# Kernel tuning notes

Hardware: AMD Instinct MI355X
Metric: run time of the kernel (lower is better)

The kernel has to match this reference:

```python
import jax, jax.numpy as jnp
import numpy as np

N_HEADS = 32
N_KV_HEADS = 8
HEAD_DIM = 128
HIDDEN = 4096
ROPE_BASE = 10000.0


def _rope_tables(seq_len, head_dim, base):
    inv_freq = 1.0 / (base ** (jnp.arange(0, head_dim, 2, dtype=jnp.float32) / head_dim))
    t = jnp.arange(seq_len, dtype=jnp.float32)
    freqs = jnp.outer(t, inv_freq)                    # (S, D/2)
    emb = jnp.concatenate([freqs, freqs], axis=-1)    # (S, D)
    return jnp.cos(emb), jnp.sin(emb)


def _rotate_half(x):
    half = x.shape[-1] // 2
    return jnp.concatenate([-x[..., half:], x[..., :half]], axis=-1)


def _apply_rope(x, cos, sin):
    # x: (B, H, S, D); cos/sin: (S, D)
    return x * cos[None, None] + _rotate_half(x) * sin[None, None]


def setup_inputs() -> dict:
    key = jax.random.key(0)
    k1, k2, k3 = jax.random.split(key, 3)
    bsz, q_len = 2, 2048
    total_heads = N_HEADS + 2 * N_KV_HEADS
    hidden_states = jax.random.normal(k1, (bsz, q_len, HIDDEN), dtype=jnp.float32)
    w_qkv = jax.random.normal(k2, (total_heads * HEAD_DIM, HIDDEN), dtype=jnp.float32) * 0.02
    w_o = jax.random.normal(k3, (HIDDEN, N_HEADS * HEAD_DIM), dtype=jnp.float32) * 0.02
    return {"hidden_states": hidden_states, "w_qkv": w_qkv, "w_o": w_o}


def reference(hidden_states, w_qkv, w_o):
    bsz, q_len, _ = hidden_states.shape
    n_rep = N_HEADS // N_KV_HEADS

    qkv = jnp.einsum('bsh,oh->bso', hidden_states, w_qkv)  # (B, S, total_heads*D)
    q_sz = N_HEADS * HEAD_DIM
    kv_sz = N_KV_HEADS * HEAD_DIM
    q = qkv[..., :q_sz].reshape(bsz, q_len, N_HEADS, HEAD_DIM).transpose(0, 2, 1, 3)
    k = qkv[..., q_sz:q_sz + kv_sz].reshape(bsz, q_len, N_KV_HEADS, HEAD_DIM).transpose(0, 2, 1, 3)
    v = qkv[..., q_sz + kv_sz:].reshape(bsz, q_len, N_KV_HEADS, HEAD_DIM).transpose(0, 2, 1, 3)

    cos, sin = _rope_tables(q_len, HEAD_DIM, ROPE_BASE)
    q = _apply_rope(q, cos, sin)
    k = _apply_rope(k, cos, sin)

    # repeat KV heads for GQA
    k = jnp.repeat(k, n_rep, axis=1)  # (B, H, S, D)
    v = jnp.repeat(v, n_rep, axis=1)

    scale = HEAD_DIM ** -0.5
    scores = jnp.einsum('bhqd,bhkd->bhqk', q, k) * scale
    causal = jnp.tril(jnp.ones((q_len, q_len), dtype=bool))
    scores = jnp.where(causal[None, None], scores, jnp.finfo(scores.dtype).min)
    attn = jax.nn.softmax(scores, axis=-1)
    out = jnp.einsum('bhqk,bhkd->bhqd', attn, v)  # (B, H, S, D)
    out = out.transpose(0, 2, 1, 3).reshape(bsz, q_len, N_HEADS * HEAD_DIM)
    return jnp.einsum('bso,ho->bsh', out, w_o)
```

## Files before the change

### kernel.cpp

```cpp
#include <hip/hip_runtime.h>
#include <stdint.h>

#define N_HEADS   32
#define N_KV      8
#define HEAD_DIM  128
#define HIDDEN_DIM 4096
#define BSZ       2
#define SEQ       2048
#define TOT_HEADS 48
#define QKV_DIM   6144
#define ROWS      4096
#define ROPE_HEADS 40

typedef __attribute__((ext_vector_type(4)))  float f32x4;
typedef __attribute__((ext_vector_type(16))) float f32x16;
typedef __attribute__((ext_vector_type(8)))  short bf16x8;
typedef unsigned short u16;
typedef unsigned int   u32;

#define AS1 __attribute__((address_space(1)))
#define AS3 __attribute__((address_space(3)))

static __device__ __forceinline__ float bf16f(u16 u) { return __uint_as_float(((u32)u) << 16); }
static __device__ __forceinline__ u16 f2bf(float f) {
  u32 x = __float_as_uint(f);
  x += 0x7fffu + ((x >> 16) & 1u);
  return (u16)(x >> 16);
}
static __device__ __forceinline__ u32 cvt_pk_bf16(float lo, float hi) {
  u32 r;
  asm("v_cvt_pk_bf16_f32 %0, %1, %2" : "=v"(r) : "v"(lo), "v"(hi));
  return r;
}
static __device__ __forceinline__ bf16x8 mk8(u32 a, u32 b, u32 c, u32 d) {
  union { u32 u[4]; bf16x8 v; } x;
  x.u[0] = a; x.u[1] = b; x.u[2] = c; x.u[3] = d;
  return x.v;
}

__global__ void cast_f32_bf16_k(const float4* __restrict__ in, ushort4* __restrict__ out, int n4) {
  int i = blockIdx.x * blockDim.x + threadIdx.x;
  const int stride = gridDim.x * blockDim.x;
  for (; i < n4; i += stride) {
    float4 v = in[i];
    ushort4 o;
    o.x = f2bf(v.x); o.y = f2bf(v.y); o.z = f2bf(v.z); o.w = f2bf(v.w);
    out[i] = o;
  }
}

__global__ void rope_tables_k(float* __restrict__ ctab, float* __restrict__ stab) {
  int t = blockIdx.x * blockDim.x + threadIdx.x;
  if (t >= SEQ * 64) return;
  int s = t >> 6, i = t & 63;
  float inv = powf(10000.0f, -(float)i / 64.0f);
  float ang = (float)s * inv;
  float sv, cv;
  sincosf(ang, &sv, &cv);
  ctab[t] = cv; stab[t] = sv;
}

template<int F32OUT>
__global__ __launch_bounds__(256, 2)
void gemm_bt_k(const u16* __restrict__ A, const u16* __restrict__ Bw,
               void* __restrict__ C, int M, int N, int K)
{
  __shared__ uint4 smA[1024];
  __shared__ uint4 smB[1024];
  const int tid = threadIdx.x;
  const int nbx = N >> 7;
  const int bm = (blockIdx.x / nbx) << 7;
  const int bn = (blockIdx.x % nbx) << 7;
  const int lane = tid & 63;
  const int wave = tid >> 6;
  const int wm = (wave >> 1) << 6;
  const int wn = (wave & 1) << 6;
  const int fr = lane & 15;
  const int fq = lane >> 4;

  f32x4 acc[4][4];
#pragma unroll
  for (int i = 0; i < 4; ++i)
#pragma unroll
    for (int j = 0; j < 4; ++j)
      acc[i][j] = {0.f, 0.f, 0.f, 0.f};

  const int gl_r = lane >> 3;
  const int gl_c = (lane & 7) ^ gl_r;

  for (int k0 = 0; k0 < K; k0 += 64) {
#pragma unroll
    for (int i = 0; i < 4; ++i) {
      const int rbase = (wave << 5) + (i << 3);
      const int row = rbase + gl_r;
      const u16* gA = A  + (size_t)(bm + row) * K + k0 + (gl_c << 3);
      const u16* gB = Bw + (size_t)(bn + row) * K + k0 + (gl_c << 3);
      __builtin_amdgcn_global_load_lds((const AS1 u32*)gA, (AS3 u32*)&smA[rbase << 3], 16, 0, 0);
      __builtin_amdgcn_global_load_lds((const AS1 u32*)gB, (AS3 u32*)&smB[rbase << 3], 16, 0, 0);
    }
    __syncthreads();
#pragma unroll
    for (int kk = 0; kk < 2; ++kk) {
      bf16x8 af[4], bfr[4];
      const int cc = (kk << 2) + fq;
#pragma unroll
      for (int m = 0; m < 4; ++m) {
        const int row = wm + (m << 4) + fr;
        af[m] = *reinterpret_cast<const bf16x8*>(&smA[(row << 3) + (cc ^ (row & 7))]);
      }
#pragma unroll
      for (int n = 0; n < 4; ++n) {
        const int row = wn + (n << 4) + fr;
        bfr[n] = *reinterpret_cast<const bf16x8*>(&smB[(row << 3) + (cc ^ (row & 7))]);
      }
#pragma unroll
      for (int m = 0; m < 4; ++m)
#pragma unroll
        for (int n = 0; n < 4; ++n)
          acc[m][n] = __builtin_amdgcn_mfma_f32_16x16x32_bf16(af[m], bfr[n], acc[m][n], 0, 0, 0);
    }
    __syncthreads();
  }

  const int col0 = bn + wn + fr;
#pragma unroll
  for (int m = 0; m < 4; ++m) {
#pragma unroll
    for (int i = 0; i < 4; ++i) {
      const int row = bm + wm + (m << 4) + (fq << 2) + i;
      if (F32OUT) {
        float* rp = reinterpret_cast<float*>(C) + (size_t)row * N + col0;
#pragma unroll
        for (int n = 0; n < 4; ++n) rp[n << 4] = acc[m][n][i];
      } else {
        u16* rp = reinterpret_cast<u16*>(C) + (size_t)row * N + col0;
#pragma unroll
        for (int n = 0; n < 4; ++n) rp[n << 4] = f2bf(acc[m][n][i]);
      }
    }
  }
}

__global__ void rope_scatter_k(const u16* __restrict__ QKV,
                               const float* __restrict__ ctab, const float* __restrict__ stab,
                               u16* __restrict__ Qo, u16* __restrict__ Ko)
{
  const int t = blockIdx.x * blockDim.x + threadIdx.x;
  const int d = t & 63;
  const int hh = (t >> 6) % ROPE_HEADS;
  const int row = t / (64 * ROPE_HEADS);
  const int b = row >> 11, sq = row & (SEQ - 1);
  const u16* src = QKV + (size_t)row * QKV_DIM + hh * HEAD_DIM;
  const float x1 = bf16f(src[d]);
  const float x2 = bf16f(src[d + 64]);
  const float c = ctab[(sq << 6) + d], sn = stab[(sq << 6) + d];
  float y1 = x1 * c - x2 * sn;
  float y2 = x2 * c + x1 * sn;
  u16* dst;
  if (hh < N_HEADS) {
    const float SC2 = 0.1275170747f;
    y1 *= SC2; y2 *= SC2;
    dst = Qo + ((size_t)(b * N_HEADS + hh) * SEQ + sq) * HEAD_DIM;
  } else {
    dst = Ko + ((size_t)(b * N_KV + (hh - N_HEADS)) * SEQ + sq) * HEAD_DIM;
  }
  dst[d] = f2bf(y1);
  dst[d + 64] = f2bf(y2);
}

__global__ __launch_bounds__(256)
void vtrans_k(const u16* __restrict__ QKV, u16* __restrict__ Vt)
{
  __shared__ u16 tile[64][72];
  const int idx = blockIdx.x;
  const int dt = idx & 1;
  const int st = (idx >> 1) & 31;
  const int kv = (idx >> 6) & 7;
  const int b  = idx >> 9;
  const int tid = threadIdx.x;
  const int s0 = st << 6, d0 = dt << 6;
  const int rl = tid >> 3, cc8 = (tid & 7) << 3;
#pragma unroll
  for (int p = 0; p < 2; ++p) {
    const int sl = rl + (p << 5);
    const u16* src = QKV + (size_t)(b * SEQ + s0 + sl) * QKV_DIM
                   + (N_HEADS + N_KV + kv) * HEAD_DIM + d0 + cc8;
    *reinterpret_cast<uint4*>(&tile[sl][cc8]) = *reinterpret_cast<const uint4*>(src);
  }
  __syncthreads();
#pragma unroll
  for (int p = 0; p < 2; ++p) {
    const int dl = rl + (p << 5);
    u16 tmp[8];
#pragma unroll
    for (int k2 = 0; k2 < 8; ++k2) tmp[k2] = tile[cc8 + k2][dl];
    u16* dst = Vt + ((size_t)(b * N_KV + kv) * HEAD_DIM + d0 + dl) * SEQ + s0 + cc8;
    *reinterpret_cast<uint4*>(dst) = *reinterpret_cast<const uint4*>(tmp);
  }
}

__global__ __launch_bounds__(256, 2)
void attn_mfma_k(const u16* __restrict__ Q, const u16* __restrict__ K,
                 const u16* __restrict__ Vt, u16* __restrict__ Out)
{
  __shared__ uint4 Ksm[2][512];
  __shared__ uint4 Vsm[2][512];
  const int tid  = threadIdx.x;
  const int lane = tid & 63;
  const int w    = tid >> 6;
  const int idx  = blockIdx.x;
  const int kvh  = idx & 7;
  const int b    = (idx >> 3) & 1;
  const int p    = idx >> 4;
  const int h    = (kvh << 2) + w;

  const int ql = lane & 31;
  const int hh = lane >> 5;

  const u16* Qh = Q  + (size_t)(b * N_HEADS + h) * SEQ * HEAD_DIM;
  const u16* Kb = K  + (size_t)(b * N_KV + kvh) * SEQ * HEAD_DIM;
  const u16* Vb = Vt + (size_t)(b * N_KV + kvh) * HEAD_DIM * SEQ;

  int koff[8];
#pragma unroll
  for (int f = 0; f < 8; ++f) koff[f] = (ql << 4) + (((f << 1) + hh) ^ (ql & 15));
  int voff0[4], voff1[4];
#pragma unroll
  for (int dblk = 0; dblk < 4; ++dblk) {
    const int d = (dblk << 5) + ql;
    voff0[dblk] = (d << 2) + (hh ^ (d & 3));
    voff1[dblk] = (d << 2) + ((2 + hh) ^ (d & 3));
  }

  auto stage = [&](int buf, int ks) {
#pragma unroll
    for (int i = 0; i < 2; ++i) {
      const int base = i * 256 + w * 64;
      const int sl = base + lane;
      const int row = sl >> 4, cs = sl & 15;
      const int g = cs ^ (row & 15);
      const u16* src = Kb + (size_t)(ks + row) * HEAD_DIM + (g << 3);
      __builtin_amdgcn_global_load_lds((const AS1 u32*)src, (AS3 u32*)&Ksm[buf][base], 16, 0, 0);
    }
#pragma unroll
    for (int i = 0; i < 2; ++i) {
      const int base = i * 256 + w * 64;
      const int sl = base + lane;
      const int d = sl >> 2, cs = sl & 3;
      const int g = cs ^ (d & 3);
      const u16* src = Vb + (size_t)d * SEQ + ks + (g << 3);
      __builtin_amdgcn_global_load_lds((const AS1 u32*)src, (AS3 u32*)&Vsm[buf][base], 16, 0, 0);
    }
  };

#pragma unroll 1
  for (int pass = 0; pass < 2; ++pass) {
    const int qi = pass ? (31 - p) : (32 + p);
    const int q0 = qi << 5;

    bf16x8 qf[8];
#pragma unroll
    for (int f = 0; f < 8; ++f)
      qf[f] = *reinterpret_cast<const bf16x8*>(Qh + (size_t)(q0 + ql) * HEAD_DIM + 16 * f + 8 * hh);

    f32x16 o[4];
#pragma unroll
    for (int dblk = 0; dblk < 4; ++dblk)
#pragma unroll
      for (int r = 0; r < 16; ++r) o[dblk][r] = 0.f;
    float m2 = -1e30f, lsum = 0.f;

    __syncthreads();
    stage(0, 0);

#pragma unroll 1
    for (int s = 0; s <= qi; ++s) {
      const int cur = s & 1;
      __syncthreads();
      if (s < qi) stage(cur ^ 1, (s + 1) << 5);

      f32x16 T;
#pragma unroll
      for (int r = 0; r < 16; ++r) T[r] = 0.f;
      __builtin_amdgcn_s_setprio(1);
#pragma unroll
      for (int f = 0; f < 8; ++f) {
        const bf16x8 kf = *reinterpret_cast<const bf16x8*>(&Ksm[cur][koff[f]]);
        T = __builtin_amdgcn_mfma_f32_32x32x16_bf16(kf, qf[f], T, 0, 0, 0);
      }
      __builtin_amdgcn_s_setprio(0);

      if (s == qi) {
#pragma unroll
        for (int r = 0; r < 16; ++r) {
          const int krow = (r & 3) + ((r >> 2) << 3) + (hh << 2);
          if (krow > ql) T[r] = -1e30f;
        }
      }
      float mt = T[0];
#pragma unroll
      for (int r = 1; r < 16; ++r) mt = fmaxf(mt, T[r]);
      mt = fmaxf(mt, __shfl_xor(mt, 32));

      if (__any(mt > m2 + 8.f)) {
        const float mnew = fmaxf(m2, mt);
        const float resc = exp2f(m2 - mnew);
        lsum *= resc;
#pragma unroll
        for (int r = 0; r < 16; ++r) {
          const int qr = (r & 3) + ((r >> 2) << 3) + (hh << 2);
          const float rr = __shfl(resc, qr);
#pragma unroll
          for (int dblk = 0; dblk < 4; ++dblk) o[dblk][r] *= rr;
        }
        m2 = mnew;
      }

      float ps = 0.f;
#pragma unroll
      for (int r = 0; r < 16; ++r) { const float pv = exp2f(T[r] - m2); T[r] = pv; ps += pv; }
      ps += __shfl_xor(ps, 32);
      lsum += ps;

      u32 pk[8], sw[8];
#pragma unroll
      for (int i = 0; i < 8; ++i) {
        pk[i] = cvt_pk_bf16(T[2 * i], T[2 * i + 1]);
        sw[i] = (u32)__shfl_xor((int)pk[i], 32);
      }
      const bf16x8 a0 = hh ? mk8(sw[2], sw[3], pk[2], pk[3])
                           : mk8(pk[0], pk[1], sw[0], sw[1]);
      const bf16x8 a1 = hh ? mk8(sw[6], sw[7], pk[6], pk[7])
                           : mk8(pk[4], pk[5], sw[4], sw[5]);

      __builtin_amdgcn_s_setprio(1);
#pragma unroll
      for (int dblk = 0; dblk < 4; ++dblk) {
        const bf16x8 va = *reinterpret_cast<const bf16x8*>(&Vsm[cur][voff0[dblk]]);
        o[dblk] = __builtin_amdgcn_mfma_f32_32x32x16_bf16(a0, va, o[dblk], 0, 0, 0);
        const bf16x8 vb2 = *reinterpret_cast<const bf16x8*>(&Vsm[cur][voff1[dblk]]);
        o[dblk] = __builtin_amdgcn_mfma_f32_32x32x16_bf16(a1, vb2, o[dblk], 0, 0, 0);
      }
      __builtin_amdgcn_s_setprio(0);
    }

    u16* Ob = Out + (size_t)(b * SEQ + q0) * HIDDEN_DIM + h * HEAD_DIM + ql;
#pragma unroll
    for (int r = 0; r < 16; ++r) {
      const int qr = (r & 3) + ((r >> 2) << 3) + (hh << 2);
      const float il = 1.0f / __shfl(lsum, qr);
      u16* rp = Ob + (size_t)qr * HIDDEN_DIM;
#pragma unroll
      for (int dblk = 0; dblk < 4; ++dblk)
        rp[dblk * 32] = f2bf(o[dblk][r] * il);
    }
  }
}

extern "C" void kernel_launch(void* const* d_in, const int* in_sizes, int n_in,
                              void* d_out, int out_size, void* d_ws, size_t ws_size,
                              hipStream_t stream)
{
  const float* hs   = (const float*)d_in[0];
  const float* wqkv = (const float*)d_in[1];
  const float* wo   = (const float*)d_in[2];
  float* out = (float*)d_out;
  char* ws = (char*)d_ws;
  size_t off = 0;
  auto alloc = [&](size_t bytes) -> void* {
    void* p = ws + off;
    off += (bytes + 255) & ~(size_t)255;
    return p;
  };
  u16* Xbf    = (u16*)alloc((size_t)ROWS * HIDDEN_DIM * 2);
  u16* Wqkvbf = (u16*)alloc((size_t)QKV_DIM * HIDDEN_DIM * 2);
  u16* Wobf   = (u16*)alloc((size_t)HIDDEN_DIM * HIDDEN_DIM * 2);
  u16* QKVbf  = (u16*)alloc((size_t)ROWS * QKV_DIM * 2);
  u16* Qbf    = (u16*)alloc((size_t)BSZ * N_HEADS * SEQ * HEAD_DIM * 2);
  u16* Kbf    = (u16*)alloc((size_t)BSZ * N_KV * SEQ * HEAD_DIM * 2);
  u16* Vtbf   = (u16*)alloc((size_t)BSZ * N_KV * SEQ * HEAD_DIM * 2);
  float* ctab = (float*)alloc((size_t)SEQ * 64 * 4);
  float* stab = (float*)alloc((size_t)SEQ * 64 * 4);
  u16* AOut   = (u16*)alloc((size_t)ROWS * HIDDEN_DIM * 2);
  if (off > ws_size) return;

  cast_f32_bf16_k<<<2048, 256, 0, stream>>>((const float4*)hs,   (ushort4*)Xbf,    ROWS * HIDDEN_DIM / 4);
  cast_f32_bf16_k<<<2048, 256, 0, stream>>>((const float4*)wqkv, (ushort4*)Wqkvbf, QKV_DIM * HIDDEN_DIM / 4);
  cast_f32_bf16_k<<<2048, 256, 0, stream>>>((const float4*)wo,   (ushort4*)Wobf,   HIDDEN_DIM * HIDDEN_DIM / 4);
  rope_tables_k<<<(SEQ * 64) / 256, 256, 0, stream>>>(ctab, stab);

  gemm_bt_k<0><<<(ROWS / 128) * (QKV_DIM / 128), 256, 0, stream>>>(Xbf, Wqkvbf, (void*)QKVbf,
                                                                   ROWS, QKV_DIM, HIDDEN_DIM);
  rope_scatter_k<<<ROWS * ROPE_HEADS * 64 / 256, 256, 0, stream>>>(QKVbf, ctab, stab, Qbf, Kbf);
  vtrans_k<<<BSZ * N_KV * (SEQ / 64) * (HEAD_DIM / 64), 256, 0, stream>>>(QKVbf, Vtbf);
  attn_mfma_k<<<BSZ * N_KV * 32, 256, 0, stream>>>(Qbf, Kbf, Vtbf, AOut);
  gemm_bt_k<1><<<(ROWS / 128) * (HIDDEN_DIM / 128), 256, 0, stream>>>(AOut, Wobf, (void*)out,
                                                                      ROWS, HIDDEN_DIM, HIDDEN_DIM);
}
```

Measured before the change: 558.3 us.

## Rewrite projection GEMMs as 256x256-tile, 4-stage pipelined kernel with XCD remap

Replaces the 128x128 single-buffered GEMM with a 512-thread 256x256-tile kernel. It uses a 4-slot LDS ring of K=32 slices with global_load_lds prefetch three steps ahead, fine-grained vmcnt waits and split A/B staging phases. Workgroup IDs are remapped across the 8 XCDs and MFMA sections are raised in priority. The goal is to hide global load latency behind MFMA and cut per-tile A/B traffic. In exchange it uses more LDS and registers per block, and the larger tiles leave fewer blocks (384 and 256) to spread over the CUs.

```diff
diff --git a/kernel.cpp b/kernel.cpp
--- a/kernel.cpp
+++ b/kernel.cpp
@@ -60,71 +60,127 @@
   ctab[t] = cv; stab[t] = sv;
 }
 
+#define VM8 asm volatile("s_waitcnt vmcnt(8)" ::: "memory")
+#define VM4 asm volatile("s_waitcnt vmcnt(4)" ::: "memory")
+#define VM0 asm volatile("s_waitcnt vmcnt(0)" ::: "memory")
+
+#define PH_EVEN(t, WAITOP, DOSTAGE)                                            \
+  {                                                                            \
+    WAITOP;                                                                    \
+    __builtin_amdgcn_sched_barrier(0);                                         \
+    __builtin_amdgcn_s_barrier();                                              \
+    __builtin_amdgcn_sched_barrier(0);                                         \
+    if (DOSTAGE) stageA((t) + 3);                                              \
+    const int slot = ((t) & 3) << 10;                                          \
+    _Pragma("unroll")                                                          \
+    for (int n = 0; n < 4; ++n)                                                \
+      bf[n] = *reinterpret_cast<const bf16x8*>(&LB[slot + bbase + (n << 6)]);  \
+    bf16x8 af[4];                                                              \
+    _Pragma("unroll")                                                          \
+    for (int m = 0; m < 4; ++m)                                                \
+      af[m] = *reinterpret_cast<const bf16x8*>(&LA[slot + abase + (m << 6)]);  \
+    __builtin_amdgcn_s_setprio(1);                                             \
+    _Pragma("unroll")                                                          \
+    for (int m = 0; m < 4; ++m)                                                \
+      _Pragma("unroll")                                                        \
+      for (int n = 0; n < 4; ++n)                                              \
+        acc[m][n] = __builtin_amdgcn_mfma_f32_16x16x32_bf16(af[m], bf[n], acc[m][n], 0, 0, 0); \
+    __builtin_amdgcn_s_setprio(0);                                             \
+  }
+
+#define PH_ODD(t, DOSTAGE)                                                     \
+  {                                                                            \
+    __builtin_amdgcn_sched_barrier(0);                                         \
+    __builtin_amdgcn_s_barrier();                                              \
+    __builtin_amdgcn_sched_barrier(0);                                         \
+    if (DOSTAGE) stageB((t) + 3);                                              \
+    const int slot = ((t) & 3) << 10;                                          \
+    bf16x8 af[4];                                                              \
+    _Pragma("unroll")                                                          \
+    for (int m = 0; m < 4; ++m)                                                \
+      af[m] = *reinterpret_cast<const bf16x8*>(&LA[slot + abase + ((4 + m) << 6)]); \
+    __builtin_amdgcn_s_setprio(1);                                             \
+    _Pragma("unroll")                                                          \
+    for (int m = 0; m < 4; ++m)                                                \
+      _Pragma("unroll")                                                        \
+      for (int n = 0; n < 4; ++n)                                              \
+        acc[4 + m][n] = __builtin_amdgcn_mfma_f32_16x16x32_bf16(af[m], bf[n], acc[4 + m][n], 0, 0, 0); \
+    __builtin_amdgcn_s_setprio(0);                                             \
+  }
+
 template<int F32OUT>
-__global__ __launch_bounds__(256, 2)
-void gemm_bt_k(const u16* __restrict__ A, const u16* __restrict__ Bw,
+__global__ __launch_bounds__(512, 2)
+void gemm256_k(const u16* __restrict__ A, const u16* __restrict__ Bw,
                void* __restrict__ C, int M, int N, int K)
 {
-  __shared__ uint4 smA[1024];
-  __shared__ uint4 smB[1024];
+  __shared__ uint4 LA[4096];
+  __shared__ uint4 LB[4096];
+  const int NT = K >> 5;
   const int tid = threadIdx.x;
-  const int nbx = N >> 7;
-  const int bm = (blockIdx.x / nbx) << 7;
-  const int bn = (blockIdx.x % nbx) << 7;
   const int lane = tid & 63;
   const int wave = tid >> 6;
-  const int wm = (wave >> 1) << 6;
-  const int wn = (wave & 1) << 6;
+  const int nbx = N >> 8;
+  const int cpx = gridDim.x >> 3;
+  const int wg  = (blockIdx.x & 7) * cpx + (blockIdx.x >> 3);
+  const int bm = (wg / nbx) << 8;
+  const int bn = (wg % nbx) << 8;
+
+  const int wm = (wave >> 2) << 7;
+  const int wn = (wave & 3) << 6;
   const int fr = lane & 15;
   const int fq = lane >> 4;
-
-  f32x4 acc[4][4];
-#pragma unroll
-  for (int i = 0; i < 4; ++i)
-#pragma unroll
-    for (int j = 0; j < 4; ++j)
-      acc[i][j] = {0.f, 0.f, 0.f, 0.f};
-
-  const int gl_r = lane >> 3;
-  const int gl_c = (lane & 7) ^ gl_r;
-
-  for (int k0 = 0; k0 < K; k0 += 64) {
-#pragma unroll
-    for (int i = 0; i < 4; ++i) {
-      const int rbase = (wave << 5) + (i << 3);
-      const int row = rbase + gl_r;
-      const u16* gA = A  + (size_t)(bm + row) * K + k0 + (gl_c << 3);
-      const u16* gB = Bw + (size_t)(bn + row) * K + k0 + (gl_c << 3);
-      __builtin_amdgcn_global_load_lds((const AS1 u32*)gA, (AS3 u32*)&smA[rbase << 3], 16, 0, 0);
-      __builtin_amdgcn_global_load_lds((const AS1 u32*)gB, (AS3 u32*)&smB[rbase << 3], 16, 0, 0);
-    }
-    __syncthreads();
-#pragma unroll
-    for (int kk = 0; kk < 2; ++kk) {
-      bf16x8 af[4], bfr[4];
-      const int cc = (kk << 2) + fq;
-#pragma unroll
-      for (int m = 0; m < 4; ++m) {
-        const int row = wm + (m << 4) + fr;
-        af[m] = *reinterpret_cast<const bf16x8*>(&smA[(row << 3) + (cc ^ (row & 7))]);
-      }
-#pragma unroll
-      for (int n = 0; n < 4; ++n) {
-        const int row = wn + (n << 4) + fr;
-        bfr[n] = *reinterpret_cast<const bf16x8*>(&smB[(row << 3) + (cc ^ (row & 7))]);
-      }
-#pragma unroll
-      for (int m = 0; m < 4; ++m)
-#pragma unroll
-        for (int n = 0; n < 4; ++n)
-          acc[m][n] = __builtin_amdgcn_mfma_f32_16x16x32_bf16(af[m], bfr[n], acc[m][n], 0, 0, 0);
-    }
-    __syncthreads();
-  }
+  const int rpos = fq ^ ((fr >> 1) & 3);
+  const int abase = ((wm + fr) << 2) + rpos;
+  const int bbase = ((wn + fr) << 2) + rpos;
+
+  const int rA = tid >> 2;
+  const int cs8 = (((tid & 3) ^ ((tid >> 3) & 3)) << 3);
+  const u16* As0 = A  + (size_t)(bm + rA) * K + cs8;
+  const u16* As1 = As0 + (size_t)128 * K;
+  const u16* Bs0 = Bw + (size_t)(bn + rA) * K + cs8;
+  const u16* Bs1 = Bs0 + (size_t)128 * K;
+  const int ldsbase = wave << 6;
+
+  f32x4 acc[8][4];
+#pragma unroll
+  for (int m = 0; m < 8; ++m)
+#pragma unroll
+    for (int n = 0; n < 4; ++n)
+      acc[m][n] = {0.f, 0.f, 0.f, 0.f};
+
+  auto stageA = [&](int t) {
+    const int slot = (t & 3) << 10;
+    __builtin_amdgcn_global_load_lds((const AS1 u32*)(As0 + (t << 5)),
+                                     (AS3 u32*)(LA + slot + ldsbase), 16, 0, 0);
+    __builtin_amdgcn_global_load_lds((const AS1 u32*)(As1 + (t << 5)),
+                                     (AS3 u32*)(LA + slot + 512 + ldsbase), 16, 0, 0);
+  };
+  auto stageB = [&](int t) {
+    const int slot = (t & 3) << 10;
+    __builtin_amdgcn_global_load_lds((const AS1 u32*)(Bs0 + (t << 5)),
+                                     (AS3 u32*)(LB + slot + ldsbase), 16, 0, 0);
+    __builtin_amdgcn_global_load_lds((const AS1 u32*)(Bs1 + (t << 5)),
+                                     (AS3 u32*)(LB + slot + 512 + ldsbase), 16, 0, 0);
+  };
+
+  stageA(0); stageB(0); stageA(1); stageB(1); stageA(2); stageB(2);
+
+  bf16x8 bf[4];
+
+#pragma unroll 1
+  for (int t = 0; t < NT - 2; ++t) {
+    const bool st = t < NT - 3;
+    PH_EVEN(t, VM8, st);
+    PH_ODD(t, st);
+  }
+  PH_EVEN(NT - 2, VM4, false);
+  PH_ODD(NT - 2, false);
+  PH_EVEN(NT - 1, VM0, false);
+  PH_ODD(NT - 1, false);
 
   const int col0 = bn + wn + fr;
 #pragma unroll
-  for (int m = 0; m < 4; ++m) {
+  for (int m = 0; m < 8; ++m) {
 #pragma unroll
     for (int i = 0; i < 4; ++i) {
       const int row = bm + wm + (m << 4) + (fq << 2) + i;
@@ -389,11 +445,11 @@
   cast_f32_bf16_k<<<2048, 256, 0, stream>>>((const float4*)wo,   (ushort4*)Wobf,   HIDDEN_DIM * HIDDEN_DIM / 4);
   rope_tables_k<<<(SEQ * 64) / 256, 256, 0, stream>>>(ctab, stab);
 
-  gemm_bt_k<0><<<(ROWS / 128) * (QKV_DIM / 128), 256, 0, stream>>>(Xbf, Wqkvbf, (void*)QKVbf,
+  gemm256_k<0><<<(ROWS / 256) * (QKV_DIM / 256), 512, 0, stream>>>(Xbf, Wqkvbf, (void*)QKVbf,
                                                                    ROWS, QKV_DIM, HIDDEN_DIM);
   rope_scatter_k<<<ROWS * ROPE_HEADS * 64 / 256, 256, 0, stream>>>(QKVbf, ctab, stab, Qbf, Kbf);
   vtrans_k<<<BSZ * N_KV * (SEQ / 64) * (HEAD_DIM / 64), 256, 0, stream>>>(QKVbf, Vtbf);
   attn_mfma_k<<<BSZ * N_KV * 32, 256, 0, stream>>>(Qbf, Kbf, Vtbf, AOut);
-  gemm_bt_k<1><<<(ROWS / 128) * (HIDDEN_DIM / 128), 256, 0, stream>>>(AOut, Wobf, (void*)out,
+  gemm256_k<1><<<(ROWS / 256) * (HIDDEN_DIM / 256), 512, 0, stream>>>(AOut, Wobf, (void*)out,
                                                                       ROWS, HIDDEN_DIM, HIDDEN_DIM);
 }
```

New measurement: 644.9 us. +15.5%, slower.

## Split attention into one q-tile per block, raise occupancy, and fuse the cast kernels

Applied to the files above, without the earlier changes.

The attention kernel no longer pairs two query tiles per block for causal load balancing. It now launches twice as many blocks, each handling one 32-row query tile, scheduled longest-first (qi = 63 - idx/16), with launch bounds raised to 4 waves per SIMD. The aim is more parallelism and better latency hiding through occupancy and dynamic scheduling, at the risk of register spilling under the tighter bound. The three fp32-to-bf16 cast launches are also merged into one kernel to cut launch overhead.

```diff
diff --git a/kernel.cpp b/kernel.cpp
--- a/kernel.cpp
+++ b/kernel.cpp
@@ -38,14 +38,22 @@
   return x.v;
 }
 
-__global__ void cast_f32_bf16_k(const float4* __restrict__ in, ushort4* __restrict__ out, int n4) {
+__global__ void cast3_k(const float4* __restrict__ a, const float4* __restrict__ b,
+                        const float4* __restrict__ c,
+                        ushort4* __restrict__ oa, ushort4* __restrict__ ob,
+                        ushort4* __restrict__ oc, int na, int nb, int nc) {
   int i = blockIdx.x * blockDim.x + threadIdx.x;
   const int stride = gridDim.x * blockDim.x;
-  for (; i < n4; i += stride) {
-    float4 v = in[i];
+  const int tot = na + nb + nc;
+  for (; i < tot; i += stride) {
+    const float4* s; ushort4* d; int j = i;
+    if (j < na)           { s = a; d = oa; }
+    else if (j < na + nb) { s = b; d = ob; j -= na; }
+    else                  { s = c; d = oc; j -= na + nb; }
+    const float4 v = s[j];
     ushort4 o;
     o.x = f2bf(v.x); o.y = f2bf(v.y); o.z = f2bf(v.z); o.w = f2bf(v.w);
-    out[i] = o;
+    d[j] = o;
   }
 }
 
@@ -199,7 +207,7 @@
   }
 }
 
-__global__ __launch_bounds__(256, 2)
+__global__ __launch_bounds__(256, 4)
 void attn_mfma_k(const u16* __restrict__ Q, const u16* __restrict__ K,
                  const u16* __restrict__ Vt, u16* __restrict__ Out)
 {
@@ -211,7 +219,8 @@
   const int idx  = blockIdx.x;
   const int kvh  = idx & 7;
   const int b    = (idx >> 3) & 1;
-  const int p    = idx >> 4;
+  const int qi   = 63 - (idx >> 4);
+  const int q0   = qi << 5;
   const int h    = (kvh << 2) + w;
 
   const int ql = lane & 31;
@@ -253,107 +262,100 @@
     }
   };
 
+  bf16x8 qf[8];
+#pragma unroll
+  for (int f = 0; f < 8; ++f)
+    qf[f] = *reinterpret_cast<const bf16x8*>(Qh + (size_t)(q0 + ql) * HEAD_DIM + 16 * f + 8 * hh);
+
+  f32x16 o[4];
+#pragma unroll
+  for (int dblk = 0; dblk < 4; ++dblk)
+#pragma unroll
+    for (int r = 0; r < 16; ++r) o[dblk][r] = 0.f;
+  float m2 = -1e30f, lsum = 0.f;
+
+  stage(0, 0);
+
 #pragma unroll 1
-  for (int pass = 0; pass < 2; ++pass) {
-    const int qi = pass ? (31 - p) : (32 + p);
-    const int q0 = qi << 5;
-
-    bf16x8 qf[8];
-#pragma unroll
-    for (int f = 0; f < 8; ++f)
-      qf[f] = *reinterpret_cast<const bf16x8*>(Qh + (size_t)(q0 + ql) * HEAD_DIM + 16 * f + 8 * hh);
-
-    f32x16 o[4];
+  for (int s = 0; s <= qi; ++s) {
+    const int cur = s & 1;
+    __syncthreads();
+    if (s < qi) stage(cur ^ 1, (s + 1) << 5);
+
+    f32x16 T;
+#pragma unroll
+    for (int r = 0; r < 16; ++r) T[r] = 0.f;
+    __builtin_amdgcn_s_setprio(1);
+#pragma unroll
+    for (int f = 0; f < 8; ++f) {
+      const bf16x8 kf = *reinterpret_cast<const bf16x8*>(&Ksm[cur][koff[f]]);
+      T = __builtin_amdgcn_mfma_f32_32x32x16_bf16(kf, qf[f], T, 0, 0, 0);
+    }
+    __builtin_amdgcn_s_setprio(0);
+
+    if (s == qi) {
+#pragma unroll
+      for (int r = 0; r < 16; ++r) {
+        const int krow = (r & 3) + ((r >> 2) << 3) + (hh << 2);
+        if (krow > ql) T[r] = -1e30f;
+      }
+    }
+    float mt = T[0];
+#pragma unroll
+    for (int r = 1; r < 16; ++r) mt = fmaxf(mt, T[r]);
+    mt = fmaxf(mt, __shfl_xor(mt, 32));
+
+    if (__any(mt > m2 + 8.f)) {
+      const float mnew = fmaxf(m2, mt);
+      const float resc = exp2f(m2 - mnew);
+      lsum *= resc;
+#pragma unroll
+      for (int r = 0; r < 16; ++r) {
+        const int qr = (r & 3) + ((r >> 2) << 3) + (hh << 2);
+        const float rr = __shfl(resc, qr);
+#pragma unroll
+        for (int dblk = 0; dblk < 4; ++dblk) o[dblk][r] *= rr;
+      }
+      m2 = mnew;
+    }
+
+    float ps = 0.f;
+#pragma unroll
+    for (int r = 0; r < 16; ++r) { const float pv = exp2f(T[r] - m2); T[r] = pv; ps += pv; }
+    ps += __shfl_xor(ps, 32);
+    lsum += ps;
+
+    u32 pk[8], sw[8];
+#pragma unroll
+    for (int i = 0; i < 8; ++i) {
+      pk[i] = cvt_pk_bf16(T[2 * i], T[2 * i + 1]);
+      sw[i] = (u32)__shfl_xor((int)pk[i], 32);
+    }
+    const bf16x8 a0 = hh ? mk8(sw[2], sw[3], pk[2], pk[3])
+                         : mk8(pk[0], pk[1], sw[0], sw[1]);
+    const bf16x8 a1 = hh ? mk8(sw[6], sw[7], pk[6], pk[7])
+                         : mk8(pk[4], pk[5], sw[4], sw[5]);
+
+    __builtin_amdgcn_s_setprio(1);
+#pragma unroll
+    for (int dblk = 0; dblk < 4; ++dblk) {
+      const bf16x8 va = *reinterpret_cast<const bf16x8*>(&Vsm[cur][voff0[dblk]]);
+      o[dblk] = __builtin_amdgcn_mfma_f32_32x32x16_bf16(a0, va, o[dblk], 0, 0, 0);
+      const bf16x8 vb2 = *reinterpret_cast<const bf16x8*>(&Vsm[cur][voff1[dblk]]);
+      o[dblk] = __builtin_amdgcn_mfma_f32_32x32x16_bf16(a1, vb2, o[dblk], 0, 0, 0);
+    }
+    __builtin_amdgcn_s_setprio(0);
+  }
+
+  u16* Ob = Out + (size_t)(b * SEQ + q0) * HIDDEN_DIM + h * HEAD_DIM + ql;
+#pragma unroll
+  for (int r = 0; r < 16; ++r) {
+    const int qr = (r & 3) + ((r >> 2) << 3) + (hh << 2);
+    const float il = 1.0f / __shfl(lsum, qr);
+    u16* rp = Ob + (size_t)qr * HIDDEN_DIM;
 #pragma unroll
     for (int dblk = 0; dblk < 4; ++dblk)
-#pragma unroll
-      for (int r = 0; r < 16; ++r) o[dblk][r] = 0.f;
-    float m2 = -1e30f, lsum = 0.f;
-
-    __syncthreads();
-    stage(0, 0);
-
-#pragma unroll 1
-    for (int s = 0; s <= qi; ++s) {
-      const int cur = s & 1;
-      __syncthreads();
-      if (s < qi) stage(cur ^ 1, (s + 1) << 5);
-
-      f32x16 T;
-#pragma unroll
-      for (int r = 0; r < 16; ++r) T[r] = 0.f;
-      __builtin_amdgcn_s_setprio(1);
-#pragma unroll
-      for (int f = 0; f < 8; ++f) {
-        const bf16x8 kf = *reinterpret_cast<const bf16x8*>(&Ksm[cur][koff[f]]);
-        T = __builtin_amdgcn_mfma_f32_32x32x16_bf16(kf, qf[f], T, 0, 0, 0);
-      }
-      __builtin_amdgcn_s_setprio(0);
-
-      if (s == qi) {
-#pragma unroll
-        for (int r = 0; r < 16; ++r) {
-          const int krow = (r & 3) + ((r >> 2) << 3) + (hh << 2);
-          if (krow > ql) T[r] = -1e30f;
-        }
-      }
-      float mt = T[0];
-#pragma unroll
-      for (int r = 1; r < 16; ++r) mt = fmaxf(mt, T[r]);
-      mt = fmaxf(mt, __shfl_xor(mt, 32));
-
-      if (__any(mt > m2 + 8.f)) {
-        const float mnew = fmaxf(m2, mt);
-        const float resc = exp2f(m2 - mnew);
-        lsum *= resc;
-#pragma unroll
-        for (int r = 0; r < 16; ++r) {
-          const int qr = (r & 3) + ((r >> 2) << 3) + (hh << 2);
-          const float rr = __shfl(resc, qr);
-#pragma unroll
-          for (int dblk = 0; dblk < 4; ++dblk) o[dblk][r] *= rr;
-        }
-        m2 = mnew;
-      }
-
-      float ps = 0.f;
-#pragma unroll
-      for (int r = 0; r < 16; ++r) { const float pv = exp2f(T[r] - m2); T[r] = pv; ps += pv; }
-      ps += __shfl_xor(ps, 32);
-      lsum += ps;
-
-      u32 pk[8], sw[8];
-#pragma unroll
-      for (int i = 0; i < 8; ++i) {
-        pk[i] = cvt_pk_bf16(T[2 * i], T[2 * i + 1]);
-        sw[i] = (u32)__shfl_xor((int)pk[i], 32);
-      }
-      const bf16x8 a0 = hh ? mk8(sw[2], sw[3], pk[2], pk[3])
-                           : mk8(pk[0], pk[1], sw[0], sw[1]);
-      const bf16x8 a1 = hh ? mk8(sw[6], sw[7], pk[6], pk[7])
-                           : mk8(pk[4], pk[5], sw[4], sw[5]);
-
-      __builtin_amdgcn_s_setprio(1);
-#pragma unroll
-      for (int dblk = 0; dblk < 4; ++dblk) {
-        const bf16x8 va = *reinterpret_cast<const bf16x8*>(&Vsm[cur][voff0[dblk]]);
-        o[dblk] = __builtin_amdgcn_mfma_f32_32x32x16_bf16(a0, va, o[dblk], 0, 0, 0);
-        const bf16x8 vb2 = *reinterpret_cast<const bf16x8*>(&Vsm[cur][voff1[dblk]]);
-        o[dblk] = __builtin_amdgcn_mfma_f32_32x32x16_bf16(a1, vb2, o[dblk], 0, 0, 0);
-      }
-      __builtin_amdgcn_s_setprio(0);
-    }
-
-    u16* Ob = Out + (size_t)(b * SEQ + q0) * HIDDEN_DIM + h * HEAD_DIM + ql;
-#pragma unroll
-    for (int r = 0; r < 16; ++r) {
-      const int qr = (r & 3) + ((r >> 2) << 3) + (hh << 2);
-      const float il = 1.0f / __shfl(lsum, qr);
-      u16* rp = Ob + (size_t)qr * HIDDEN_DIM;
-#pragma unroll
-      for (int dblk = 0; dblk < 4; ++dblk)
-        rp[dblk * 32] = f2bf(o[dblk][r] * il);
-    }
+      rp[dblk * 32] = f2bf(o[dblk][r] * il);
   }
 }
 
@@ -384,16 +386,17 @@
   u16* AOut   = (u16*)alloc((size_t)ROWS * HIDDEN_DIM * 2);
   if (off > ws_size) return;
 
-  cast_f32_bf16_k<<<2048, 256, 0, stream>>>((const float4*)hs,   (ushort4*)Xbf,    ROWS * HIDDEN_DIM / 4);
-  cast_f32_bf16_k<<<2048, 256, 0, stream>>>((const float4*)wqkv, (ushort4*)Wqkvbf, QKV_DIM * HIDDEN_DIM / 4);
-  cast_f32_bf16_k<<<2048, 256, 0, stream>>>((const float4*)wo,   (ushort4*)Wobf,   HIDDEN_DIM * HIDDEN_DIM / 4);
+  cast3_k<<<4096, 256, 0, stream>>>((const float4*)hs, (const float4*)wqkv, (const float4*)wo,
+                                    (ushort4*)Xbf, (ushort4*)Wqkvbf, (ushort4*)Wobf,
+                                    ROWS * HIDDEN_DIM / 4, QKV_DIM * HIDDEN_DIM / 4,
+                                    HIDDEN_DIM * HIDDEN_DIM / 4);
   rope_tables_k<<<(SEQ * 64) / 256, 256, 0, stream>>>(ctab, stab);
 
   gemm_bt_k<0><<<(ROWS / 128) * (QKV_DIM / 128), 256, 0, stream>>>(Xbf, Wqkvbf, (void*)QKVbf,
                                                                    ROWS, QKV_DIM, HIDDEN_DIM);
   rope_scatter_k<<<ROWS * ROPE_HEADS * 64 / 256, 256, 0, stream>>>(QKVbf, ctab, stab, Qbf, Kbf);
   vtrans_k<<<BSZ * N_KV * (SEQ / 64) * (HEAD_DIM / 64), 256, 0, stream>>>(QKVbf, Vtbf);
-  attn_mfma_k<<<BSZ * N_KV * 32, 256, 0, stream>>>(Qbf, Kbf, Vtbf, AOut);
+  attn_mfma_k<<<BSZ * N_KV * 64, 256, 0, stream>>>(Qbf, Kbf, Vtbf, AOut);
   gemm_bt_k<1><<<(ROWS / 128) * (HIDDEN_DIM / 128), 256, 0, stream>>>(AOut, Wobf, (void*)out,
                                                                       ROWS, HIDDEN_DIM, HIDDEN_DIM);
 }
```

Measured after the change: 686.2 us. 1.23x slower.
